# Kernel optimization log

Hardware: AMD Instinct MI355X
Metric: run time of the kernel (lower is better)

The kernel has to match this reference:

```python
import jax, jax.numpy as jnp
import numpy as np

L_LIST = [0, 1, 2, 3]
PAIRS = [(l1, l2) for l1 in L_LIST for l2 in L_LIST if l1 <= l2]
S, I, N = 8, 32, 8  # structures, atoms per structure, radial functions


def setup_inputs() -> dict:
    key = jax.random.key(0)
    inp = {}
    for l in L_LIST:
        key, k1, k2 = jax.random.split(key, 3)
        inp[f"c_in_l{l}"] = jax.random.normal(k1, (S, I, 2 * l + 1, N), dtype=jnp.float32)
        inp[f"c_tgt_l{l}"] = jax.random.normal(k2, (S, I, 2 * l + 1, N), dtype=jnp.float32)
    for (l1, l2) in PAIRS:
        key, k1 = jax.random.split(key)
        # overlap block stored pre-permuted: [S, i1, m1, n1, i2, m2, n2]
        inp[f"ovlp_l{l1}_l{l2}"] = jax.random.normal(
            k1, (S, I, 2 * l1 + 1, N, I, 2 * l2 + 1, N), dtype=jnp.float32)
    return inp


def _rho_loss(c_in, c_tgt, ovlp):
    # delta_coeffs = input - target, per (l) block (single species)
    d = {l: c_in[l] - c_tgt[l] for l in L_LIST}
    total = jnp.float32(0.0)
    for (l1, l2) in PAIRS:
        O = ovlp[(l1, l2)]
        # tensordot(c1, O, dims=3) over (i1, m1, n1), batched over structures s
        t = jnp.einsum('simn,simnjpq->sjpq', d[l1], O)
        # tensordot(t, c2, dims=3) over (i2, m2, n2), then sum over structures
        b = jnp.einsum('sjpq,sjpq->', t, d[l2])
        # diagonal blocks (l1==l2, a1==a2) counted once, off-diagonal twice
        total = total + (b if l1 == l2 else 2.0 * b)
    return total


def reference(c_in_l0, c_tgt_l0, c_in_l1, c_tgt_l1, c_in_l2, c_tgt_l2,
              c_in_l3, c_tgt_l3, ovlp_l0_l0, ovlp_l0_l1, ovlp_l0_l2,
              ovlp_l0_l3, ovlp_l1_l1, ovlp_l1_l2, ovlp_l1_l3, ovlp_l2_l2,
              ovlp_l2_l3, ovlp_l3_l3):
    c_in = {0: c_in_l0, 1: c_in_l1, 2: c_in_l2, 3: c_in_l3}
    c_tgt = {0: c_tgt_l0, 1: c_tgt_l1, 2: c_tgt_l2, 3: c_tgt_l3}
    ovlp = {(0, 0): ovlp_l0_l0, (0, 1): ovlp_l0_l1, (0, 2): ovlp_l0_l2,
            (0, 3): ovlp_l0_l3, (1, 1): ovlp_l1_l1, (1, 2): ovlp_l1_l2,
            (1, 3): ovlp_l1_l3, (2, 2): ovlp_l2_l2, (2, 3): ovlp_l2_l3,
            (3, 3): ovlp_l3_l3}
    return _rho_loss(c_in, c_tgt, ovlp)
```

## Files before the change

### kernel.cpp

```cpp
#include <hip/hip_runtime.h>


#define NUM_S 8

typedef float vfloat4 __attribute__((ext_vector_type(4)));

__device__ float g_d[32768];

__global__ __launch_bounds__(256) void compute_d_kernel(
    const float* __restrict__ ci0, const float* __restrict__ ct0,
    const float* __restrict__ ci1, const float* __restrict__ ct1,
    const float* __restrict__ ci2, const float* __restrict__ ct2,
    const float* __restrict__ ci3, const float* __restrict__ ct3) {
    const int t = blockIdx.x * 256 + threadIdx.x;
    float v;
    if (t < 2048)       v = ci0[t]         - ct0[t];
    else if (t < 8192)  v = ci1[t - 2048]  - ct1[t - 2048];
    else if (t < 18432) v = ci2[t - 8192]  - ct2[t - 8192];
    else                v = ci3[t - 18432] - ct3[t - 18432];
    g_d[t] = v;
}

template <int K1, int K2, int W, int NWP>
__device__ __forceinline__ float pair_rows(const float* __restrict__ O,
                                           const float* __restrict__ d1,
                                           const float* __restrict__ d2,
                                           int lw, int lane) {
    constexpr int C2q    = K2 / 4;
    constexpr int ROUNDS = C2q / 64;
    constexpr int NROWS  = NUM_S * K1;

    const int r_beg = (int)(((long long)lw * NROWS) / NWP);
    const int r_end = (int)(((long long)(lw + 1) * NROWS) / NWP);

    const vfloat4* __restrict__ O4 = (const vfloat4*)O;

    float ax = 0.f, ay = 0.f, az = 0.f, aw = 0.f;
    for (int t = r_beg; t < r_end; ++t) {
        const int s = t / K1;
        const vfloat4* __restrict__ o = O4 + (size_t)t * C2q + lane;
        const vfloat4* __restrict__ v = (const vfloat4*)(d2 + s * K2) + lane;

        vfloat4 ov[ROUNDS], vv[ROUNDS];
#pragma unroll
        for (int j = 0; j < ROUNDS; ++j)
            ov[j] = __builtin_nontemporal_load(o + j * 64);
#pragma unroll
        for (int j = 0; j < ROUNDS; ++j) vv[j] = v[j * 64];

        const float dd = d1[t];

        float dx = 0.f, dy = 0.f, dz = 0.f, dw = 0.f;
#pragma unroll
        for (int j = 0; j < ROUNDS; ++j) {
            dx = fmaf(ov[j].x, vv[j].x, dx);
            dy = fmaf(ov[j].y, vv[j].y, dy);
            dz = fmaf(ov[j].z, vv[j].z, dz);
            dw = fmaf(ov[j].w, vv[j].w, dw);
        }
        ax = fmaf(dd, dx, ax);
        ay = fmaf(dd, dy, ay);
        az = fmaf(dd, dz, az);
        aw = fmaf(dd, dw, aw);
    }
    return (float)W * ((ax + ay) + (az + aw));
}

__global__ __launch_bounds__(256) void rho_loss_kernel(
    const float* __restrict__ O00, const float* __restrict__ O01,
    const float* __restrict__ O02, const float* __restrict__ O03,
    const float* __restrict__ O11, const float* __restrict__ O12,
    const float* __restrict__ O13, const float* __restrict__ O22,
    const float* __restrict__ O23, const float* __restrict__ O33,
    float* __restrict__ out) {
    const int lane = threadIdx.x & 63;
    const int wid  = blockIdx.x * 4 + (threadIdx.x >> 6);

    const float* D0 = g_d;
    const float* D1 = g_d + 2048;
    const float* D2 = g_d + 8192;
    const float* D3 = g_d + 18432;

    float acc;
    if      (wid <   47) acc = pair_rows< 256,  256, 1,   47>(O00, D0, D0, wid,        lane);
    else if (wid <  192) acc = pair_rows< 256,  768, 2,  145>(O01, D0, D1, wid -   47, lane);
    else if (wid <  433) acc = pair_rows< 256, 1280, 2,  241>(O02, D0, D2, wid -  192, lane);
    else if (wid <  770) acc = pair_rows< 256, 1792, 2,  337>(O03, D0, D3, wid -  433, lane);
    else if (wid < 1204) acc = pair_rows< 768,  768, 1,  434>(O11, D1, D1, wid -  770, lane);
    else if (wid < 1927) acc = pair_rows< 768, 1280, 2,  723>(O12, D1, D2, wid - 1204, lane);
    else if (wid < 2939) acc = pair_rows< 768, 1792, 2, 1012>(O13, D1, D3, wid - 1927, lane);
    else if (wid < 4144) acc = pair_rows<1280, 1280, 1, 1205>(O22, D2, D2, wid - 2939, lane);
    else if (wid < 5831) acc = pair_rows<1280, 1792, 2, 1687>(O23, D2, D3, wid - 4144, lane);
    else                 acc = pair_rows<1792, 1792, 1, 2361>(O33, D3, D3, wid - 5831, lane);

    for (int off = 32; off > 0; off >>= 1)
        acc += __shfl_down(acc, off, 64);

    __shared__ float wsum[4];
    const int lwid = threadIdx.x >> 6;
    if (lane == 0) wsum[lwid] = acc;
    __syncthreads();
    if (threadIdx.x == 0) {
        float s = wsum[0] + wsum[1] + wsum[2] + wsum[3];
        atomicAdd(out, s);
    }
}

extern "C" void kernel_launch(void* const* d_in, const int* in_sizes, int n_in,
                              void* d_out, int out_size, void* d_ws, size_t ws_size,
                              hipStream_t stream) {
    (void)in_sizes; (void)n_in; (void)d_ws; (void)ws_size; (void)out_size;

    const float* ci0 = (const float*)d_in[0];
    const float* ct0 = (const float*)d_in[1];
    const float* ci1 = (const float*)d_in[2];
    const float* ct1 = (const float*)d_in[3];
    const float* ci2 = (const float*)d_in[4];
    const float* ct2 = (const float*)d_in[5];
    const float* ci3 = (const float*)d_in[6];
    const float* ct3 = (const float*)d_in[7];
    const float* O00 = (const float*)d_in[8];
    const float* O01 = (const float*)d_in[9];
    const float* O02 = (const float*)d_in[10];
    const float* O03 = (const float*)d_in[11];
    const float* O11 = (const float*)d_in[12];
    const float* O12 = (const float*)d_in[13];
    const float* O13 = (const float*)d_in[14];
    const float* O22 = (const float*)d_in[15];
    const float* O23 = (const float*)d_in[16];
    const float* O33 = (const float*)d_in[17];

    hipMemsetAsync(d_out, 0, sizeof(float), stream);

    compute_d_kernel<<<128, 256, 0, stream>>>(ci0, ct0, ci1, ct1,
                                              ci2, ct2, ci3, ct3);

    rho_loss_kernel<<<2048, 256, 0, stream>>>(
        O00, O01, O02, O03, O11, O12, O13, O22, O23, O33, (float*)d_out);
}
```

Baseline: 319.4 us.

## Use atomic work-stealing over finer row units and fold output zeroing into prep kernel

Splits the overlap contraction into twice as many, smaller work units and has each wavefront fetch further units from a global atomic counter after its statically assigned first unit, so load balances across waves. The output memset is removed and the output and counter are reset inside the d-computation kernel. This aims to reduce tail imbalance and one launch/memset, at the cost of per-unit atomic traffic and a serial dependency between unit fetches.

```diff
diff --git a/kernel.cpp b/kernel.cpp
--- a/kernel.cpp
+++ b/kernel.cpp
@@ -6,13 +6,19 @@
 typedef float vfloat4 __attribute__((ext_vector_type(4)));
 
 __device__ float g_d[32768];
+__device__ unsigned g_ctr;
+
+#define NV  16384u
+#define NPW 8192u
 
 __global__ __launch_bounds__(256) void compute_d_kernel(
     const float* __restrict__ ci0, const float* __restrict__ ct0,
     const float* __restrict__ ci1, const float* __restrict__ ct1,
     const float* __restrict__ ci2, const float* __restrict__ ct2,
-    const float* __restrict__ ci3, const float* __restrict__ ct3) {
+    const float* __restrict__ ci3, const float* __restrict__ ct3,
+    float* __restrict__ out) {
     const int t = blockIdx.x * 256 + threadIdx.x;
+    if (t == 0) { *out = 0.0f; g_ctr = NPW; }
     float v;
     if (t < 2048)       v = ci0[t]         - ct0[t];
     else if (t < 8192)  v = ci1[t - 2048]  - ct1[t - 2048];
@@ -66,6 +72,30 @@
     return (float)W * ((ax + ay) + (az + aw));
 }
 
+__device__ __forceinline__ float do_unit(
+    unsigned v, int lane,
+    const float* __restrict__ O00, const float* __restrict__ O01,
+    const float* __restrict__ O02, const float* __restrict__ O03,
+    const float* __restrict__ O11, const float* __restrict__ O12,
+    const float* __restrict__ O13, const float* __restrict__ O22,
+    const float* __restrict__ O23, const float* __restrict__ O33) {
+    const float* D0 = g_d;
+    const float* D1 = g_d + 2048;
+    const float* D2 = g_d + 8192;
+    const float* D3 = g_d + 18432;
+
+    if      (v <    94u) return pair_rows< 256,  256, 1,   94>(O00, D0, D0, (int)v,           lane);
+    else if (v <   384u) return pair_rows< 256,  768, 2,  290>(O01, D0, D1, (int)(v -    94), lane);
+    else if (v <   866u) return pair_rows< 256, 1280, 2,  482>(O02, D0, D2, (int)(v -   384), lane);
+    else if (v <  1540u) return pair_rows< 256, 1792, 2,  674>(O03, D0, D3, (int)(v -   866), lane);
+    else if (v <  2408u) return pair_rows< 768,  768, 1,  868>(O11, D1, D1, (int)(v -  1540), lane);
+    else if (v <  3854u) return pair_rows< 768, 1280, 2, 1446>(O12, D1, D2, (int)(v -  2408), lane);
+    else if (v <  5878u) return pair_rows< 768, 1792, 2, 2024>(O13, D1, D3, (int)(v -  3854), lane);
+    else if (v <  8288u) return pair_rows<1280, 1280, 1, 2410>(O22, D2, D2, (int)(v -  5878), lane);
+    else if (v < 11662u) return pair_rows<1280, 1792, 2, 3374>(O23, D2, D3, (int)(v -  8288), lane);
+    else                 return pair_rows<1792, 1792, 1, 4722>(O33, D3, D3, (int)(v - 11662), lane);
+}
+
 __global__ __launch_bounds__(256) void rho_loss_kernel(
     const float* __restrict__ O00, const float* __restrict__ O01,
     const float* __restrict__ O02, const float* __restrict__ O03,
@@ -74,24 +104,19 @@
     const float* __restrict__ O23, const float* __restrict__ O33,
     float* __restrict__ out) {
     const int lane = threadIdx.x & 63;
-    const int wid  = blockIdx.x * 4 + (threadIdx.x >> 6);
+    const unsigned pw = blockIdx.x * 4 + (threadIdx.x >> 6);
 
-    const float* D0 = g_d;
-    const float* D1 = g_d + 2048;
-    const float* D2 = g_d + 8192;
-    const float* D3 = g_d + 18432;
+    float acc = 0.f;
+    unsigned v = pw;
+    while (v < NV) {
+        unsigned nv = 0xffffffffu;
+        if (lane == 0) nv = atomicAdd(&g_ctr, 1u);
 
-    float acc;
-    if      (wid <   47) acc = pair_rows< 256,  256, 1,   47>(O00, D0, D0, wid,        lane);
-    else if (wid <  192) acc = pair_rows< 256,  768, 2,  145>(O01, D0, D1, wid -   47, lane);
-    else if (wid <  433) acc = pair_rows< 256, 1280, 2,  241>(O02, D0, D2, wid -  192, lane);
-    else if (wid <  770) acc = pair_rows< 256, 1792, 2,  337>(O03, D0, D3, wid -  433, lane);
-    else if (wid < 1204) acc = pair_rows< 768,  768, 1,  434>(O11, D1, D1, wid -  770, lane);
-    else if (wid < 1927) acc = pair_rows< 768, 1280, 2,  723>(O12, D1, D2, wid - 1204, lane);
-    else if (wid < 2939) acc = pair_rows< 768, 1792, 2, 1012>(O13, D1, D3, wid - 1927, lane);
-    else if (wid < 4144) acc = pair_rows<1280, 1280, 1, 1205>(O22, D2, D2, wid - 2939, lane);
-    else if (wid < 5831) acc = pair_rows<1280, 1792, 2, 1687>(O23, D2, D3, wid - 4144, lane);
-    else                 acc = pair_rows<1792, 1792, 1, 2361>(O33, D3, D3, wid - 5831, lane);
+        acc += do_unit(v, lane, O00, O01, O02, O03, O11, O12, O13,
+                       O22, O23, O33);
+
+        v = (unsigned)__shfl((int)nv, 0, 64);
+    }
 
     for (int off = 32; off > 0; off >>= 1)
         acc += __shfl_down(acc, off, 64);
@@ -130,10 +155,9 @@
     const float* O23 = (const float*)d_in[16];
     const float* O33 = (const float*)d_in[17];
 
-    hipMemsetAsync(d_out, 0, sizeof(float), stream);
-
     compute_d_kernel<<<128, 256, 0, stream>>>(ci0, ct0, ci1, ct1,
-                                              ci2, ct2, ci3, ct3);
+                                              ci2, ct2, ci3, ct3,
+                                              (float*)d_out);
 
     rho_loss_kernel<<<2048, 256, 0, stream>>>(
         O00, O01, O02, O03, O11, O12, O13, O22, O23, O33, (float*)d_out);
```

Result: slower. 609.9 us (+90.9%).
